# Performance work log

Hardware: AMD Instinct MI355X
Metric: run time of the kernel (lower is better)

The kernel has to match this reference:

```python
import jax, jax.numpy as jnp
import numpy as np

NUM_HEADS = 16
ROPE_BASE = 10000.0


def _rope_cos_sin(seq_len, head_dim, dtype):
    inv_freq = 1.0 / (ROPE_BASE ** (jnp.arange(0, head_dim, 2, dtype=jnp.float32) / head_dim))
    t = jnp.arange(seq_len, dtype=jnp.float32)
    freqs = t[:, None] * inv_freq[None, :]          # [S, hd/2]
    emb = jnp.concatenate([freqs, freqs], axis=-1)  # [S, hd]
    return jnp.cos(emb).astype(dtype), jnp.sin(emb).astype(dtype)


def _rotate_half(x):
    x1, x2 = jnp.split(x, 2, axis=-1)
    return jnp.concatenate([-x2, x1], axis=-1)


def setup_inputs() -> dict:
    key = jax.random.key(0)
    k1, k2, k3 = jax.random.split(key, 3)
    B, S, D = 4, 2048, 1024
    x = jax.random.normal(k1, (B, S, D), dtype=jnp.float32)
    w_qkv = jax.random.normal(k2, (3 * D, D), dtype=jnp.float32) * (D ** -0.5)
    w_out = jax.random.normal(k3, (D, D), dtype=jnp.float32) * (D ** -0.5)
    return {"x": x, "w_qkv": w_qkv, "w_out": w_out}


def reference(x, w_qkv, w_out):
    B, S, D = x.shape
    H = NUM_HEADS
    hd = D // H
    scale = hd ** -0.5

    qkv = jnp.einsum('bsd,ed->bse', x, w_qkv)           # [B, S, 3D]
    qkv = qkv.reshape(B, S, 3, H, hd).transpose(2, 0, 3, 1, 4)  # [3, B, H, S, hd]
    q, k, v = qkv[0], qkv[1], qkv[2]

    cos, sin = _rope_cos_sin(S, hd, x.dtype)            # [S, hd] broadcast over B,H
    q = q * cos + _rotate_half(q) * sin
    k = k * cos + _rotate_half(k) * sin

    scores = jnp.einsum('bhqd,bhkd->bhqk', q, k) * scale  # [B, H, S, S]
    causal = jnp.tril(jnp.ones((S, S), dtype=bool))
    scores = jnp.where(causal, scores, jnp.finfo(scores.dtype).min)
    attn = jax.nn.softmax(scores, axis=-1)

    out = jnp.einsum('bhqk,bhkd->bhqd', attn, v)        # [B, H, S, hd]
    out = out.transpose(0, 2, 1, 3).reshape(B, S, D)
    out = jnp.einsum('bsd,ed->bse', out, w_out)
    return out
```

## Files before the change

kernel.cpp:

```cpp
#include <hip/hip_runtime.h>
#include <hip/hip_bf16.h>

typedef __bf16 bf16x8 __attribute__((ext_vector_type(8)));
typedef float f32x4 __attribute__((ext_vector_type(4)));
typedef __hip_bfloat16 bf16;

#define B_ 4
#define S_ 2048
#define D_ 1024
#define H_ 16
#define HD_ 64

__device__ __forceinline__ void gload16(const bf16* g, bf16* l) {
  __builtin_amdgcn_global_load_lds(
      (const __attribute__((address_space(1))) unsigned int*)g,
      (__attribute__((address_space(3))) unsigned int*)l, 16, 0, 0);
}

#define NX_ (B_ * S_ * D_)
#define NW1_ (3 * D_ * D_)
#define NW2_ (D_ * D_)
__global__ __launch_bounds__(256) void k_cvt3(const float* __restrict__ x,
                                              const float* __restrict__ w1,
                                              const float* __restrict__ w2,
                                              bf16* __restrict__ ox,
                                              bf16* __restrict__ o1,
                                              bf16* __restrict__ o2) {
  int i = (blockIdx.x * 256 + threadIdx.x) * 4;
  const float* in;
  bf16* out;
  if (i < NX_) {
    in = x; out = ox;
  } else if (i < NX_ + NW1_) {
    in = w1; out = o1; i -= NX_;
  } else {
    in = w2; out = o2; i -= NX_ + NW1_;
  }
  float4 v = *reinterpret_cast<const float4*>(in + i);
  alignas(8) bf16 t[4];
  t[0] = __float2bfloat16(v.x);
  t[1] = __float2bfloat16(v.y);
  t[2] = __float2bfloat16(v.z);
  t[3] = __float2bfloat16(v.w);
  *reinterpret_cast<uint2*>(out + i) = *reinterpret_cast<uint2*>(t);
}

__global__ __launch_bounds__(512) void k_qkv(const bf16* __restrict__ X,
                                             const bf16* __restrict__ W,
                                             bf16* __restrict__ Qw,
                                             bf16* __restrict__ Kw,
                                             bf16* __restrict__ Vtw) {
  __shared__ bf16 Al[2][128 * 64];
  __shared__ bf16 Bl[2][256 * 64];
  const int tid = threadIdx.x;
  const int wid = tid >> 6, lane = tid & 63, col = lane & 15, g = lane >> 4;
  const int wr = wid >> 2, wc = wid & 3;
  const int m0 = blockIdx.x * 128, n0 = blockIdx.y * 256;
  const int srow = tid >> 3;
  const int scol = (tid & 7) * 8;
  const int csrc = scol ^ ((srow & 7) * 8);
  const bf16* ga = X + (size_t)(m0 + srow) * 1024 + csrc;
  const bf16* gb = W + (size_t)(n0 + srow) * 1024 + csrc;
  const int ldst = srow * 64 + scol;
  const int rsw = (col & 7) * 8;
  f32x4 acc[4][4] = {};
#define QKV_STAGE(buf, k0)                                   \
  do {                                                       \
    gload16(ga + (k0), &Al[buf][ldst]);                      \
    gload16(ga + (k0) + 64 * 1024, &Al[buf][ldst + 4096]);   \
    gload16(gb + (k0), &Bl[buf][ldst]);                      \
    gload16(gb + (k0) + 64 * 1024, &Bl[buf][ldst + 4096]);   \
    gload16(gb + (k0) + 128 * 1024, &Bl[buf][ldst + 8192]);  \
    gload16(gb + (k0) + 192 * 1024, &Bl[buf][ldst + 12288]); \
  } while (0)
  QKV_STAGE(0, 0);
  QKV_STAGE(1, 64);
  for (int kt = 0; kt < 16; ++kt) {
    const int c = kt & 1;
    if (kt < 15)
      asm volatile("s_waitcnt vmcnt(6)" ::: "memory");
    else
      asm volatile("s_waitcnt vmcnt(0)" ::: "memory");
    __builtin_amdgcn_s_barrier();
    const bf16* Ac = Al[c];
    const bf16* Bc = Bl[c];
#pragma unroll
    for (int kk = 0; kk < 2; ++kk) {
      const int ce = (kk * 32 + g * 8) ^ rsw;
      bf16x8 af[4], bfr[4];
#pragma unroll
      for (int m = 0; m < 4; ++m)
        af[m] = *reinterpret_cast<const bf16x8*>(&Ac[(wr * 64 + m * 16 + col) * 64 + ce]);
#pragma unroll
      for (int n = 0; n < 4; ++n)
        bfr[n] =
            *reinterpret_cast<const bf16x8*>(&Bc[(wc * 64 + n * 16 + col) * 64 + ce]);
      __builtin_amdgcn_s_setprio(1);
#pragma unroll
      for (int m = 0; m < 4; ++m)
#pragma unroll
        for (int n = 0; n < 4; ++n)
          acc[m][n] =
              __builtin_amdgcn_mfma_f32_16x16x32_bf16(af[m], bfr[n], acc[m][n], 0, 0, 0);
      __builtin_amdgcn_s_setprio(0);
    }
    __builtin_amdgcn_s_barrier();
    if (kt + 2 < 16) QKV_STAGE(c, (kt + 2) * 64);
  }
#undef QKV_STAGE
  const int e0 = n0 + wc * 64;
  const int which = e0 >> 10;
  const int h = (e0 >> 6) & 15;
  if (which == 2) {
#pragma unroll
    for (int m = 0; m < 4; ++m) {
      int mg = m0 + wr * 64 + m * 16 + g * 4;
      int b = mg >> 11, s = mg & 2047;
#pragma unroll
      for (int n = 0; n < 4; ++n) {
        int d = n * 16 + col;
        alignas(8) bf16 t[4];
#pragma unroll
        for (int r = 0; r < 4; ++r) t[r] = __float2bfloat16(acc[m][n][r]);
        *reinterpret_cast<uint2*>(&Vtw[((size_t)((b * 16 + h) * 64 + d) << 11) + s]) =
            *reinterpret_cast<uint2*>(t);
      }
    }
  } else {
    bf16* dst = which ? Kw : Qw;
    const float scale = which ? 1.0f : 0.18033688011112042f;
    const float fexp = -2.0f * 13.287712379549449f / 64.0f;
#pragma unroll
    for (int i = 0; i < 2; ++i) {
      int dlo = i * 16 + col;
      float invf = exp2f(fexp * (float)dlo);
#pragma unroll
      for (int m = 0; m < 4; ++m) {
        int mg = m0 + wr * 64 + m * 16 + g * 4;
        int b = mg >> 11;
        size_t rb = (size_t)(b * 16 + h) << 11;
#pragma unroll
        for (int r = 0; r < 4; ++r) {
          int s = (mg + r) & 2047;
          float sn, cs;
          __sincosf((float)s * invf, &sn, &cs);
          float lo = acc[m][i][r] * scale, hi = acc[m][i + 2][r] * scale;
          dst[((rb + s) << 6) + dlo] = __float2bfloat16(lo * cs - hi * sn);
          dst[((rb + s) << 6) + dlo + 32] = __float2bfloat16(hi * cs + lo * sn);
        }
      }
    }
  }
}

__global__ __launch_bounds__(512) void k_attn(const bf16* __restrict__ Q,
                                              const bf16* __restrict__ K,
                                              const bf16* __restrict__ Vt,
                                              bf16* __restrict__ AO) {
  __shared__ bf16 QPl[128][72];
  __shared__ bf16 Kl[64][72];
  __shared__ bf16 Vl[64][72];
  const int tid = threadIdx.x;
  const int wave = tid >> 6, lane = tid & 63, col = lane & 15, g = lane >> 4;
  const int bh = blockIdx.x;
  const size_t base = (size_t)bh << 17;
  const int r0 = tid >> 3, c0 = (tid & 7) * 8;
  const int b = bh >> 4, h = bh & 15;
  const int yy = blockIdx.y, a = yy >> 2, r_ = yy & 3;
  const int qt = (a == 0) ? (15 - r_) : (a == 1) ? (8 + (r_ ^ 2)) : (a == 2) ? (4 + (r_ ^ 1)) : r_;
  const int q0 = qt * 128;
  *reinterpret_cast<int4*>(&QPl[r0][c0]) =
      *reinterpret_cast<const int4*>(&Q[base + (size_t)(q0 + r0) * 64 + c0]);
  *reinterpret_cast<int4*>(&QPl[r0 + 64][c0]) =
      *reinterpret_cast<const int4*>(&Q[base + (size_t)(q0 + r0 + 64) * 64 + c0]);
  const int ktlim = 2 * qt + 1;
  const int ktmax = (q0 + wave * 16 + 15) >> 6;
  int4 kr = *reinterpret_cast<const int4*>(&K[base + (size_t)r0 * 64 + c0]);
  int4 vr = *reinterpret_cast<const int4*>(&Vt[base + (size_t)r0 * 2048 + c0]);
  *reinterpret_cast<int4*>(&Kl[r0][c0]) = kr;
  *reinterpret_cast<int4*>(&Vl[r0][c0]) = vr;
  kr = *reinterpret_cast<const int4*>(&K[base + (size_t)(64 + r0) * 64 + c0]);
  vr = *reinterpret_cast<const int4*>(&Vt[base + (size_t)r0 * 2048 + 64 + c0]);
  __syncthreads();
  bf16x8 qf[2];
#pragma unroll
  for (int kk = 0; kk < 2; ++kk)
    qf[kk] = *reinterpret_cast<const bf16x8*>(&QPl[wave * 16 + col][g * 8 + kk * 32]);
  float l_s = 0.0f;
  f32x4 o[4] = {};
  for (int kt = 0; kt <= ktlim; ++kt) {
    const int k0 = kt * 64;
    if (kt <= ktmax) {
      const int q = q0 + wave * 16 + col;
      const bool needmask = (k0 + 63 > q0 + wave * 16);
      __builtin_amdgcn_s_setprio(1);
#pragma unroll
      for (int n = 0; n < 4; ++n) {
        f32x4 s = {};
#pragma unroll
        for (int kk = 0; kk < 2; ++kk) {
          bf16x8 kf =
              *reinterpret_cast<const bf16x8*>(&Kl[n * 16 + col][g * 8 + kk * 32]);
          s = __builtin_amdgcn_mfma_f32_16x16x32_bf16(kf, qf[kk], s, 0, 0, 0);
        }
        if (needmask) {
#pragma unroll
          for (int r = 0; r < 4; ++r)
            if (k0 + n * 16 + g * 4 + r > q) s[r] = -3e38f;
        }
        alignas(8) bf16 t[4];
#pragma unroll
        for (int r = 0; r < 4; ++r) {
          float p = exp2f(s[r]);
          l_s += p;
          t[r] = __float2bfloat16(p);
        }
        *reinterpret_cast<uint2*>(&QPl[wave * 16 + col][n * 16 + g * 4]) =
            *reinterpret_cast<uint2*>(t);
      }
#pragma unroll
      for (int kk = 0; kk < 2; ++kk) {
        bf16x8 pf =
            *reinterpret_cast<const bf16x8*>(&QPl[wave * 16 + col][g * 8 + kk * 32]);
#pragma unroll
        for (int n2 = 0; n2 < 4; ++n2) {
          bf16x8 vf =
              *reinterpret_cast<const bf16x8*>(&Vl[n2 * 16 + col][g * 8 + kk * 32]);
          o[n2] = __builtin_amdgcn_mfma_f32_16x16x32_bf16(pf, vf, o[n2], 0, 0, 0);
        }
      }
      __builtin_amdgcn_s_setprio(0);
    }
    __syncthreads();
    if (kt < ktlim) {
      *reinterpret_cast<int4*>(&Kl[r0][c0]) = kr;
      *reinterpret_cast<int4*>(&Vl[r0][c0]) = vr;
      if (kt + 2 <= ktlim) {
        const int k2 = k0 + 128;
        kr = *reinterpret_cast<const int4*>(&K[base + (size_t)(k2 + r0) * 64 + c0]);
        vr = *reinterpret_cast<const int4*>(&Vt[base + (size_t)r0 * 2048 + k2 + c0]);
      }
      __syncthreads();
    }
  }
  l_s += __shfl_xor(l_s, 16);
  l_s += __shfl_xor(l_s, 32);
#pragma unroll
  for (int r = 0; r < 4; ++r) {
    float inv = 1.0f / __shfl(l_s, (lane & 48) | (g * 4 + r));
    int s = q0 + wave * 16 + g * 4 + r;
#pragma unroll
    for (int n2 = 0; n2 < 4; ++n2)
      AO[((size_t)(b * 2048 + s) << 10) + h * 64 + n2 * 16 + col] =
          __float2bfloat16(o[n2][r] * inv);
  }
}

__global__ __launch_bounds__(512) void k_outproj(const bf16* __restrict__ A,
                                                 const bf16* __restrict__ W,
                                                 float* __restrict__ OUT) {
  __shared__ bf16 Al[2][128 * 64];
  __shared__ bf16 Bl[2][256 * 64];
  const int tid = threadIdx.x;
  const int wid = tid >> 6, lane = tid & 63, col = lane & 15, g = lane >> 4;
  const int wr = wid >> 2, wc = wid & 3;
  const int m0 = blockIdx.x * 128, n0 = blockIdx.y * 256;
  const int srow = tid >> 3;
  const int scol = (tid & 7) * 8;
  const int csrc = scol ^ ((srow & 7) * 8);
  const bf16* ga = A + (size_t)(m0 + srow) * 1024 + csrc;
  const bf16* gb = W + (size_t)(n0 + srow) * 1024 + csrc;
  const int ldst = srow * 64 + scol;
  const int rsw = (col & 7) * 8;
  f32x4 acc[4][4] = {};
#define OP_STAGE(buf, k0)                                    \
  do {                                                       \
    gload16(ga + (k0), &Al[buf][ldst]);                      \
    gload16(ga + (k0) + 64 * 1024, &Al[buf][ldst + 4096]);   \
    gload16(gb + (k0), &Bl[buf][ldst]);                      \
    gload16(gb + (k0) + 64 * 1024, &Bl[buf][ldst + 4096]);   \
    gload16(gb + (k0) + 128 * 1024, &Bl[buf][ldst + 8192]);  \
    gload16(gb + (k0) + 192 * 1024, &Bl[buf][ldst + 12288]); \
  } while (0)
  OP_STAGE(0, 0);
  OP_STAGE(1, 64);
  for (int kt = 0; kt < 16; ++kt) {
    const int c = kt & 1;
    if (kt < 15)
      asm volatile("s_waitcnt vmcnt(6)" ::: "memory");
    else
      asm volatile("s_waitcnt vmcnt(0)" ::: "memory");
    __builtin_amdgcn_s_barrier();
    const bf16* Ac = Al[c];
    const bf16* Bc = Bl[c];
#pragma unroll
    for (int kk = 0; kk < 2; ++kk) {
      const int ce = (kk * 32 + g * 8) ^ rsw;
      bf16x8 af[4], bfr[4];
#pragma unroll
      for (int m = 0; m < 4; ++m)
        af[m] = *reinterpret_cast<const bf16x8*>(&Ac[(wr * 64 + m * 16 + col) * 64 + ce]);
#pragma unroll
      for (int n = 0; n < 4; ++n)
        bfr[n] =
            *reinterpret_cast<const bf16x8*>(&Bc[(wc * 64 + n * 16 + col) * 64 + ce]);
      __builtin_amdgcn_s_setprio(1);
#pragma unroll
      for (int m = 0; m < 4; ++m)
#pragma unroll
        for (int n = 0; n < 4; ++n)
          acc[m][n] =
              __builtin_amdgcn_mfma_f32_16x16x32_bf16(af[m], bfr[n], acc[m][n], 0, 0, 0);
      __builtin_amdgcn_s_setprio(0);
    }
    __builtin_amdgcn_s_barrier();
    if (kt + 2 < 16) OP_STAGE(c, (kt + 2) * 64);
  }
#undef OP_STAGE
#pragma unroll
  for (int m = 0; m < 4; ++m)
#pragma unroll
    for (int n = 0; n < 4; ++n)
#pragma unroll
      for (int r = 0; r < 4; ++r)
        OUT[(size_t)(m0 + wr * 64 + m * 16 + g * 4 + r) * 1024 + n0 + wc * 64 + n * 16 +
            col] = acc[m][n][r];
}

extern "C" void kernel_launch(void* const* d_in, const int* in_sizes, int n_in,
                              void* d_out, int out_size, void* d_ws, size_t ws_size,
                              hipStream_t stream) {
  const float* x = (const float*)d_in[0];
  const float* wqkv = (const float*)d_in[1];
  const float* wout = (const float*)d_in[2];
  float* out = (float*)d_out;

  char* ws = (char*)d_ws;
  const size_t SZ_X = (size_t)B_ * S_ * D_ * 2;
  const size_t SZ_WQKV = (size_t)3 * D_ * D_ * 2;
  const size_t SZ_WOUT = (size_t)D_ * D_ * 2;
  const size_t SZ_T = (size_t)B_ * H_ * S_ * HD_ * 2;
  bf16* xb = (bf16*)(ws);
  bf16* wqkvb = (bf16*)(ws + SZ_X);
  bf16* woutb = (bf16*)(ws + SZ_X + SZ_WQKV);
  bf16* qws = (bf16*)(ws + SZ_X + SZ_WQKV + SZ_WOUT);
  bf16* kws = (bf16*)(ws + SZ_X + SZ_WQKV + SZ_WOUT + SZ_T);
  bf16* vtws = (bf16*)(ws + SZ_X + SZ_WQKV + SZ_WOUT + 2 * SZ_T);
  bf16* aob = (bf16*)(ws + SZ_X + SZ_WQKV + SZ_WOUT + 3 * SZ_T);

  const int NTOT4 = (NX_ + NW1_ + NW2_) / 4;
  k_cvt3<<<NTOT4 / 256, 256, 0, stream>>>(x, wqkv, wout, xb, wqkvb, woutb);

  k_qkv<<<dim3(64, 12), 512, 0, stream>>>(xb, wqkvb, qws, kws, vtws);
  k_attn<<<dim3(B_ * H_, 16), 512, 0, stream>>>(qws, kws, vtws, aob);
  k_outproj<<<dim3(64, 4), 512, 0, stream>>>(aob, woutb, out);
}
```

Baseline: 176.3 us.

## Interleave next-tile global-to-LDS loads with MFMA clusters in GEMM kernels

In both the QKV projection and output projection GEMMs, all LDS fragments for the whole 64-wide k-tile are now read into registers up front. The MFMAs are split into four clusters, and the next stage's global_load_lds issues are spread between those clusters after an early barrier. Before, the loads were issued in one burst after all compute. The aim is to overlap memory issue with matrix math and shorten the barrier-to-barrier critical path. The cost is higher register pressure from holding two k-slices of fragments, plus an extra lgkmcnt wait.

```diff
diff --git a/kernel.cpp b/kernel.cpp
--- a/kernel.cpp
+++ b/kernel.cpp
@@ -16,6 +16,8 @@
       (const __attribute__((address_space(1))) unsigned int*)g,
       (__attribute__((address_space(3))) unsigned int*)l, 16, 0, 0);
 }
+
+#define MFMA16(a, b, c) __builtin_amdgcn_mfma_f32_16x16x32_bf16((a), (b), (c), 0, 0, 0)
 
 #define NX_ (B_ * S_ * D_)
 #define NW1_ (3 * D_ * D_)
@@ -64,7 +66,7 @@
   const int ldst = srow * 64 + scol;
   const int rsw = (col & 7) * 8;
   f32x4 acc[4][4] = {};
-#define QKV_STAGE(buf, k0)                                   \
+#define QKV_STAGE_ALL(buf, k0)                               \
   do {                                                       \
     gload16(ga + (k0), &Al[buf][ldst]);                      \
     gload16(ga + (k0) + 64 * 1024, &Al[buf][ldst + 4096]);   \
@@ -73,8 +75,8 @@
     gload16(gb + (k0) + 128 * 1024, &Bl[buf][ldst + 8192]);  \
     gload16(gb + (k0) + 192 * 1024, &Bl[buf][ldst + 12288]); \
   } while (0)
-  QKV_STAGE(0, 0);
-  QKV_STAGE(1, 64);
+  QKV_STAGE_ALL(0, 0);
+  QKV_STAGE_ALL(1, 64);
   for (int kt = 0; kt < 16; ++kt) {
     const int c = kt & 1;
     if (kt < 15)
@@ -84,30 +86,66 @@
     __builtin_amdgcn_s_barrier();
     const bf16* Ac = Al[c];
     const bf16* Bc = Bl[c];
+    bf16x8 af[2][4], bfr[2][4];
 #pragma unroll
     for (int kk = 0; kk < 2; ++kk) {
       const int ce = (kk * 32 + g * 8) ^ rsw;
-      bf16x8 af[4], bfr[4];
 #pragma unroll
       for (int m = 0; m < 4; ++m)
-        af[m] = *reinterpret_cast<const bf16x8*>(&Ac[(wr * 64 + m * 16 + col) * 64 + ce]);
+        af[kk][m] =
+            *reinterpret_cast<const bf16x8*>(&Ac[(wr * 64 + m * 16 + col) * 64 + ce]);
 #pragma unroll
       for (int n = 0; n < 4; ++n)
-        bfr[n] =
+        bfr[kk][n] =
             *reinterpret_cast<const bf16x8*>(&Bc[(wc * 64 + n * 16 + col) * 64 + ce]);
-      __builtin_amdgcn_s_setprio(1);
-#pragma unroll
-      for (int m = 0; m < 4; ++m)
-#pragma unroll
-        for (int n = 0; n < 4; ++n)
-          acc[m][n] =
-              __builtin_amdgcn_mfma_f32_16x16x32_bf16(af[m], bfr[n], acc[m][n], 0, 0, 0);
-      __builtin_amdgcn_s_setprio(0);
-    }
+    }
+    __builtin_amdgcn_s_setprio(1);
+#pragma unroll
+    for (int m = 0; m < 4; ++m) {
+      acc[m][0] = MFMA16(af[0][m], bfr[0][0], acc[m][0]);
+      acc[m][1] = MFMA16(af[0][m], bfr[0][1], acc[m][1]);
+    }
+    __builtin_amdgcn_s_setprio(0);
+    asm volatile("s_waitcnt lgkmcnt(0)" ::: "memory");
+    __builtin_amdgcn_sched_barrier(0);
     __builtin_amdgcn_s_barrier();
-    if (kt + 2 < 16) QKV_STAGE(c, (kt + 2) * 64);
-  }
-#undef QKV_STAGE
+    const bool more = (kt + 2 < 16);
+    const int k2 = (kt + 2) * 64;
+    if (more) {
+      gload16(ga + k2, &Al[c][ldst]);
+      gload16(ga + k2 + 64 * 1024, &Al[c][ldst + 4096]);
+    }
+    __builtin_amdgcn_s_setprio(1);
+#pragma unroll
+    for (int m = 0; m < 4; ++m) {
+      acc[m][2] = MFMA16(af[0][m], bfr[0][2], acc[m][2]);
+      acc[m][3] = MFMA16(af[0][m], bfr[0][3], acc[m][3]);
+    }
+    __builtin_amdgcn_s_setprio(0);
+    if (more) {
+      gload16(gb + k2, &Bl[c][ldst]);
+      gload16(gb + k2 + 64 * 1024, &Bl[c][ldst + 4096]);
+    }
+    __builtin_amdgcn_s_setprio(1);
+#pragma unroll
+    for (int m = 0; m < 4; ++m) {
+      acc[m][0] = MFMA16(af[1][m], bfr[1][0], acc[m][0]);
+      acc[m][1] = MFMA16(af[1][m], bfr[1][1], acc[m][1]);
+    }
+    __builtin_amdgcn_s_setprio(0);
+    if (more) {
+      gload16(gb + k2 + 128 * 1024, &Bl[c][ldst + 8192]);
+      gload16(gb + k2 + 192 * 1024, &Bl[c][ldst + 12288]);
+    }
+    __builtin_amdgcn_s_setprio(1);
+#pragma unroll
+    for (int m = 0; m < 4; ++m) {
+      acc[m][2] = MFMA16(af[1][m], bfr[1][2], acc[m][2]);
+      acc[m][3] = MFMA16(af[1][m], bfr[1][3], acc[m][3]);
+    }
+    __builtin_amdgcn_s_setprio(0);
+  }
+#undef QKV_STAGE_ALL
   const int e0 = n0 + wc * 64;
   const int which = e0 >> 10;
   const int h = (e0 >> 6) & 15;
@@ -201,7 +239,7 @@
         for (int kk = 0; kk < 2; ++kk) {
           bf16x8 kf =
               *reinterpret_cast<const bf16x8*>(&Kl[n * 16 + col][g * 8 + kk * 32]);
-          s = __builtin_amdgcn_mfma_f32_16x16x32_bf16(kf, qf[kk], s, 0, 0, 0);
+          s = MFMA16(kf, qf[kk], s);
         }
         if (needmask) {
 #pragma unroll
@@ -226,7 +264,7 @@
         for (int n2 = 0; n2 < 4; ++n2) {
           bf16x8 vf =
               *reinterpret_cast<const bf16x8*>(&Vl[n2 * 16 + col][g * 8 + kk * 32]);
-          o[n2] = __builtin_amdgcn_mfma_f32_16x16x32_bf16(pf, vf, o[n2], 0, 0, 0);
+          o[n2] = MFMA16(pf, vf, o[n2]);
         }
       }
       __builtin_amdgcn_s_setprio(0);
@@ -273,7 +311,7 @@
   const int ldst = srow * 64 + scol;
   const int rsw = (col & 7) * 8;
   f32x4 acc[4][4] = {};
-#define OP_STAGE(buf, k0)                                    \
+#define OP_STAGE_ALL(buf, k0)                                \
   do {                                                       \
     gload16(ga + (k0), &Al[buf][ldst]);                      \
     gload16(ga + (k0) + 64 * 1024, &Al[buf][ldst + 4096]);   \
@@ -282,8 +320,8 @@
     gload16(gb + (k0) + 128 * 1024, &Bl[buf][ldst + 8192]);  \
     gload16(gb + (k0) + 192 * 1024, &Bl[buf][ldst + 12288]); \
   } while (0)
-  OP_STAGE(0, 0);
-  OP_STAGE(1, 64);
+  OP_STAGE_ALL(0, 0);
+  OP_STAGE_ALL(1, 64);
   for (int kt = 0; kt < 16; ++kt) {
     const int c = kt & 1;
     if (kt < 15)
@@ -293,30 +331,66 @@
     __builtin_amdgcn_s_barrier();
     const bf16* Ac = Al[c];
     const bf16* Bc = Bl[c];
+    bf16x8 af[2][4], bfr[2][4];
 #pragma unroll
     for (int kk = 0; kk < 2; ++kk) {
       const int ce = (kk * 32 + g * 8) ^ rsw;
-      bf16x8 af[4], bfr[4];
 #pragma unroll
       for (int m = 0; m < 4; ++m)
-        af[m] = *reinterpret_cast<const bf16x8*>(&Ac[(wr * 64 + m * 16 + col) * 64 + ce]);
+        af[kk][m] =
+            *reinterpret_cast<const bf16x8*>(&Ac[(wr * 64 + m * 16 + col) * 64 + ce]);
 #pragma unroll
       for (int n = 0; n < 4; ++n)
-        bfr[n] =
+        bfr[kk][n] =
             *reinterpret_cast<const bf16x8*>(&Bc[(wc * 64 + n * 16 + col) * 64 + ce]);
-      __builtin_amdgcn_s_setprio(1);
-#pragma unroll
-      for (int m = 0; m < 4; ++m)
-#pragma unroll
-        for (int n = 0; n < 4; ++n)
-          acc[m][n] =
-              __builtin_amdgcn_mfma_f32_16x16x32_bf16(af[m], bfr[n], acc[m][n], 0, 0, 0);
-      __builtin_amdgcn_s_setprio(0);
-    }
+    }
+    __builtin_amdgcn_s_setprio(1);
+#pragma unroll
+    for (int m = 0; m < 4; ++m) {
+      acc[m][0] = MFMA16(af[0][m], bfr[0][0], acc[m][0]);
+      acc[m][1] = MFMA16(af[0][m], bfr[0][1], acc[m][1]);
+    }
+    __builtin_amdgcn_s_setprio(0);
+    asm volatile("s_waitcnt lgkmcnt(0)" ::: "memory");
+    __builtin_amdgcn_sched_barrier(0);
     __builtin_amdgcn_s_barrier();
-    if (kt + 2 < 16) OP_STAGE(c, (kt + 2) * 64);
-  }
-#undef OP_STAGE
+    const bool more = (kt + 2 < 16);
+    const int k2 = (kt + 2) * 64;
+    if (more) {
+      gload16(ga + k2, &Al[c][ldst]);
+      gload16(ga + k2 + 64 * 1024, &Al[c][ldst + 4096]);
+    }
+    __builtin_amdgcn_s_setprio(1);
+#pragma unroll
+    for (int m = 0; m < 4; ++m) {
+      acc[m][2] = MFMA16(af[0][m], bfr[0][2], acc[m][2]);
+      acc[m][3] = MFMA16(af[0][m], bfr[0][3], acc[m][3]);
+    }
+    __builtin_amdgcn_s_setprio(0);
+    if (more) {
+      gload16(gb + k2, &Bl[c][ldst]);
+      gload16(gb + k2 + 64 * 1024, &Bl[c][ldst + 4096]);
+    }
+    __builtin_amdgcn_s_setprio(1);
+#pragma unroll
+    for (int m = 0; m < 4; ++m) {
+      acc[m][0] = MFMA16(af[1][m], bfr[1][0], acc[m][0]);
+      acc[m][1] = MFMA16(af[1][m], bfr[1][1], acc[m][1]);
+    }
+    __builtin_amdgcn_s_setprio(0);
+    if (more) {
+      gload16(gb + k2 + 128 * 1024, &Bl[c][ldst + 8192]);
+      gload16(gb + k2 + 192 * 1024, &Bl[c][ldst + 12288]);
+    }
+    __builtin_amdgcn_s_setprio(1);
+#pragma unroll
+    for (int m = 0; m < 4; ++m) {
+      acc[m][2] = MFMA16(af[1][m], bfr[1][2], acc[m][2]);
+      acc[m][3] = MFMA16(af[1][m], bfr[1][3], acc[m][3]);
+    }
+    __builtin_amdgcn_s_setprio(0);
+  }
+#undef OP_STAGE_ALL
 #pragma unroll
   for (int m = 0; m < 4; ++m)
 #pragma unroll
```

Result: faster. 160.8 us (-8.8%).
